# Kernel optimization log

Hardware: AMD Instinct MI355X
Metric: run time of the kernel (lower is better)

## Reference

```python
import jax, jax.numpy as jnp
import numpy as np

B, L, D, H = 2, 2048, 1024, 16
HD = D // H
SCALE = HD ** -0.5


def setup_inputs() -> dict:
    key = jax.random.key(0)
    ks = jax.random.split(key, 11)
    s = D ** -0.5  # torch Linear default init scale (uniform bound)
    return {
        "q": jax.random.normal(ks[0], (B, L, D), jnp.float32),
        "k": jax.random.normal(ks[1], (B, L, D), jnp.float32),
        "v": jax.random.normal(ks[2], (B, L, D), jnp.float32),
        "Wq": jax.random.uniform(ks[3], (D, D), jnp.float32, -s, s),
        "bq": jax.random.uniform(ks[4], (D,), jnp.float32, -s, s),
        "Wk": jax.random.uniform(ks[5], (D, D), jnp.float32, -s, s),
        "bk": jax.random.uniform(ks[6], (D,), jnp.float32, -s, s),
        "Wv": jax.random.uniform(ks[7], (D, D), jnp.float32, -s, s),
        "bv": jax.random.uniform(ks[8], (D,), jnp.float32, -s, s),
        "Wo": jax.random.uniform(ks[9], (D, D), jnp.float32, -s, s),
        "bo": jax.random.uniform(ks[10], (D,), jnp.float32, -s, s),
    }


def reference(q, k, v, Wq, bq, Wk, bk, Wv, bv, Wo, bo):
    b, q_len, _ = q.shape
    # projections; weights stored as (D, D) acting on the right: x @ W + b
    qh = (q @ Wq + bq).reshape(b, q_len, H, HD).transpose(0, 2, 1, 3)  # (B,H,Q,hd)
    kh = (k @ Wk + bk).reshape(b, -1, H, HD).transpose(0, 2, 1, 3)    # (B,H,K,hd)
    vh = (v @ Wv + bv).reshape(b, -1, H, HD).transpose(0, 2, 1, 3)    # (B,H,K,hd)
    att = jnp.einsum("bhqd,bhkd->bhqk", qh * SCALE, kh)               # (B,H,Q,K)
    att = jax.nn.softmax(att, axis=-1)
    out = jnp.einsum("bhqk,bhkd->bhqd", att, vh)                      # (B,H,Q,hd)
    out = out.transpose(0, 2, 1, 3).reshape(b, q_len, D)
    return out @ Wo + bo
```

## Files before the change

### kernel.cpp

```cpp
#include <hip/hip_runtime.h>

namespace {
constexpr int kB  = 2;
constexpr int kL  = 2048;
constexpr int kD  = 1024;
constexpr int kH  = 16;
constexpr int kHD = 64;
constexpr int kM  = kB * kL;
}

typedef _Float16 f16x8 __attribute__((ext_vector_type(8)));
typedef float    f32x16 __attribute__((ext_vector_type(16)));
typedef unsigned int u32;

union Frag16 { uint4 u4; unsigned u[4]; f16x8 v; };

__device__ __forceinline__ unsigned short f2h(float f) {
    return __builtin_bit_cast(unsigned short, (_Float16)f);
}
__device__ __forceinline__ unsigned pk2(float a, float b) {
    return __builtin_bit_cast(unsigned, __builtin_amdgcn_cvt_pkrtz(a, b));
}

__device__ __forceinline__ void gload16(const void* g, void* l) {
    __builtin_amdgcn_global_load_lds(
        (const __attribute__((address_space(1))) u32*)g,
        (__attribute__((address_space(3))) u32*)(unsigned long long)(__builtin_bit_cast(unsigned long long, l)),
        16, 0, 0);
}

__global__ __launch_bounds__(256) void prep_kernel(
    const float* __restrict__ q, const float* __restrict__ k,
    const float* __restrict__ v, unsigned short* __restrict__ dstA,
    const float* __restrict__ W0, const float* __restrict__ W1,
    const float* __restrict__ W2, const float* __restrict__ W3,
    unsigned short* __restrict__ WtBase)
{
    __shared__ _Float16 T[64][68];
    const int id = blockIdx.x;
    if (id < 6144) {
        const int yy = id >> 11;
        const int xx = id & 2047;
        const float* src = yy == 0 ? q : (yy == 1 ? k : v);
        unsigned short* d = dstA + (size_t)yy * ((size_t)kM * kD);
        const size_t i = ((size_t)xx * 256 + threadIdx.x) * 8;
        const float4 f0 = *(const float4*)(src + i);
        const float4 f1 = *(const float4*)(src + i + 4);
        _Float16 h[8];
        h[0] = (_Float16)f0.x; h[1] = (_Float16)f0.y;
        h[2] = (_Float16)f0.z; h[3] = (_Float16)f0.w;
        h[4] = (_Float16)f1.x; h[5] = (_Float16)f1.y;
        h[6] = (_Float16)f1.z; h[7] = (_Float16)f1.w;
        *(uint4*)(d + i) = *(uint4*)h;
        return;
    }
    const int id2 = id - 6144;
    const int z = id2 >> 8;
    const int rem = id2 & 255;
    const int by = rem >> 4, bx = rem & 15;
    const float* W = z == 0 ? W0 : z == 1 ? W1 : z == 2 ? W2 : W3;
    unsigned short* Wt = WtBase + (size_t)z * ((size_t)kD * kD);
    const int k0 = by * 64, n0 = bx * 64;
    const int tx = threadIdx.x & 15, ty = threadIdx.x >> 4;
#pragma unroll
    for (int i = 0; i < 4; ++i) {
        const int kk = i * 16 + ty;
        const float4 w = *(const float4*)&W[(size_t)(k0 + kk) * kD + n0 + tx * 4];
        T[tx * 4 + 0][kk] = (_Float16)w.x;
        T[tx * 4 + 1][kk] = (_Float16)w.y;
        T[tx * 4 + 2][kk] = (_Float16)w.z;
        T[tx * 4 + 3][kk] = (_Float16)w.w;
    }
    __syncthreads();
#pragma unroll
    for (int i = 0; i < 4; ++i) {
        const int nn = i * 16 + ty;
        *(ushort4*)&Wt[(size_t)(n0 + nn) * kD + k0 + tx * 4] = *(ushort4*)&T[nn][tx * 4];
    }
}

__global__ __launch_bounds__(256) void gemm_qkv_kernel(
    const unsigned short* __restrict__ A, const unsigned short* __restrict__ Wt,
    const float* __restrict__ bq, const float* __restrict__ bk,
    const float* __restrict__ bv, unsigned short* __restrict__ Qh,
    unsigned short* __restrict__ Kh, unsigned short* __restrict__ Vt)
{
    __shared__ unsigned short Als[2][128 * 64];
    __shared__ unsigned short Bls[2][128 * 64];

    const int tid = threadIdx.x;
    const int lane = tid & 63;
    const int wid = tid >> 6;
    const int l31 = lane & 31;
    const int hi = lane >> 5;
    const int by = blockIdx.x & 31;
    const int bxp = blockIdx.x >> 5;
    const int proj = bxp >> 3;
    const int bx = bxp & 7;
    const int row0 = by * 128;
    const int col0 = bx * 128;
    const int wr = wid >> 1, wc = wid & 1;

    const int rl = lane >> 3;
    const int sl = lane & 7;
    const int ssrc = (sl ^ rl) * 8;

    const unsigned short* Aproj = A + (size_t)proj * ((size_t)kM * kD);
    const unsigned short* Wproj = Wt + (size_t)proj * ((size_t)kD * kD);
    const unsigned short* Abase = Aproj + (size_t)(row0 + wid * 32 + rl) * kD + ssrc;
    const unsigned short* Bbase = Wproj + (size_t)(col0 + wid * 32 + rl) * kD + ssrc;

    f32x16 acc00{}, acc01{}, acc10{}, acc11{};

    auto stage = [&](int kt, int buf) {
#pragma unroll
        for (int i = 0; i < 4; ++i) {
            gload16(Abase + (size_t)(i * 8) * kD + kt * 64,
                    &Als[buf][(wid * 32 + i * 8) * 64]);
        }
#pragma unroll
        for (int i = 0; i < 4; ++i) {
            gload16(Bbase + (size_t)(i * 8) * kD + kt * 64,
                    &Bls[buf][(wid * 32 + i * 8) * 64]);
        }
    };

    const int ra0 = wr * 64 + l31;
    const int cb0 = wc * 64 + l31;

    stage(0, 0);
    int cur = 0;
    for (int kt = 0; kt < kD / 64; ++kt) {
        __syncthreads();
        if (kt + 1 < kD / 64) stage(kt + 1, cur ^ 1);
#pragma unroll
        for (int ks = 0; ks < 4; ++ks) {
            const int slot = (ks << 1) | hi;
            Frag16 a0, a1, b0, b1;
            a0.u4 = *(const uint4*)&Als[cur][ra0 * 64 + ((slot ^ (ra0 & 7)) << 3)];
            a1.u4 = *(const uint4*)&Als[cur][(ra0 + 32) * 64 + ((slot ^ ((ra0 + 32) & 7)) << 3)];
            b0.u4 = *(const uint4*)&Bls[cur][cb0 * 64 + ((slot ^ (cb0 & 7)) << 3)];
            b1.u4 = *(const uint4*)&Bls[cur][(cb0 + 32) * 64 + ((slot ^ ((cb0 + 32) & 7)) << 3)];
            acc00 = __builtin_amdgcn_mfma_f32_32x32x16_f16(a0.v, b0.v, acc00, 0, 0, 0);
            acc01 = __builtin_amdgcn_mfma_f32_32x32x16_f16(a0.v, b1.v, acc01, 0, 0, 0);
            acc10 = __builtin_amdgcn_mfma_f32_32x32x16_f16(a1.v, b0.v, acc10, 0, 0, 0);
            acc11 = __builtin_amdgcn_mfma_f32_32x32x16_f16(a1.v, b1.v, acc11, 0, 0, 0);
        }
        cur ^= 1;
    }

    const float* bias = proj == 0 ? bq : (proj == 1 ? bk : bv);
    const float bias0 = bias[col0 + wc * 64 + l31];
    const float bias1 = bias[col0 + wc * 64 + 32 + l31];
    const float oscale = proj == 0 ? (0.125f * 1.44269504089f) : 1.0f;

    const f32x16* accs[2][2] = {{&acc00, &acc01}, {&acc10, &acc11}};
#pragma unroll
    for (int rt = 0; rt < 2; ++rt) {
#pragma unroll
        for (int ct = 0; ct < 2; ++ct) {
            const f32x16& acv = *accs[rt][ct];
            const float bb = ct ? bias1 : bias0;
            const int c = col0 + wc * 64 + ct * 32 + l31;
            if (proj == 2) {
#pragma unroll
                for (int qd = 0; qd < 4; ++qd) {
                    const int r = row0 + wr * 64 + rt * 32 + 8 * qd + 4 * hi;
                    const int b_ = r >> 11;
                    int l_ = r & (kL - 1);
                    l_ ^= ((((l_ >> 2) ^ (l_ >> 3)) & 1) ? 12 : 0);
                    ushort4 w;
                    w.x = f2h(acv[4 * qd + 0] + bb);
                    w.y = f2h(acv[4 * qd + 1] + bb);
                    w.z = f2h(acv[4 * qd + 2] + bb);
                    w.w = f2h(acv[4 * qd + 3] + bb);
                    *(ushort4*)&Vt[((size_t)(b_ * kH + (c >> 6)) * kHD + (c & 63)) * kL + l_] = w;
                }
            } else {
                unsigned short* C = proj == 0 ? Qh : Kh;
#pragma unroll
                for (int reg = 0; reg < 16; ++reg) {
                    const int r = row0 + wr * 64 + rt * 32 + (reg & 3) + 8 * (reg >> 2) + 4 * hi;
                    const int b_ = r >> 11, l_ = r & (kL - 1);
                    C[((size_t)(b_ * kH + (c >> 6)) * kL + l_) * kHD + (c & 63)] =
                        f2h((acv[reg] + bb) * oscale);
                }
            }
        }
    }
}

__global__ __launch_bounds__(256) void gemm_o_kernel(
    const unsigned short* __restrict__ A, const unsigned short* __restrict__ Wt,
    const float* __restrict__ bias, float* __restrict__ C)
{
    __shared__ unsigned short Als[2][128 * 64];
    __shared__ unsigned short Bls[2][64 * 64];

    const int tid = threadIdx.x;
    const int lane = tid & 63;
    const int wid = tid >> 6;
    const int l31 = lane & 31;
    const int hi = lane >> 5;
    const int by = blockIdx.x & 31;
    const int bx = blockIdx.x >> 5;
    const int row0 = by * 128;
    const int wr = wid >> 1, wc = wid & 1;

    const int rl = lane >> 3;
    const int sl = lane & 7;
    const int ssrc = (sl ^ rl) * 8;

    const unsigned short* Abase = A + (size_t)(row0 + wid * 32 + rl) * kD + ssrc;
    const unsigned short* Bbase = Wt + (size_t)(bx * 64 + wid * 16 + rl) * kD + ssrc;

    f32x16 acc0{}, acc1{};

    auto stage = [&](int kt, int buf) {
#pragma unroll
        for (int i = 0; i < 4; ++i)
            gload16(Abase + (size_t)(i * 8) * kD + kt * 64,
                    &Als[buf][(wid * 32 + i * 8) * 64]);
        gload16(Bbase + kt * 64,                   &Bls[buf][(wid * 16) * 64]);
        gload16(Bbase + (size_t)8 * kD + kt * 64,  &Bls[buf][(wid * 16 + 8) * 64]);
    };

    const int ra0 = wr * 64 + l31;
    const int cb0 = wc * 32 + l31;

    stage(0, 0);
    int cur = 0;
    for (int kt = 0; kt < kD / 64; ++kt) {
        __syncthreads();
        if (kt + 1 < kD / 64) stage(kt + 1, cur ^ 1);
#pragma unroll
        for (int ks = 0; ks < 4; ++ks) {
            const int slot = (ks << 1) | hi;
            Frag16 a0, a1, b0;
            a0.u4 = *(const uint4*)&Als[cur][ra0 * 64 + ((slot ^ (ra0 & 7)) << 3)];
            a1.u4 = *(const uint4*)&Als[cur][(ra0 + 32) * 64 + ((slot ^ ((ra0 + 32) & 7)) << 3)];
            b0.u4 = *(const uint4*)&Bls[cur][cb0 * 64 + ((slot ^ (cb0 & 7)) << 3)];
            acc0 = __builtin_amdgcn_mfma_f32_32x32x16_f16(a0.v, b0.v, acc0, 0, 0, 0);
            acc1 = __builtin_amdgcn_mfma_f32_32x32x16_f16(a1.v, b0.v, acc1, 0, 0, 0);
        }
        cur ^= 1;
    }

    const int c = (bx << 6) + wc * 32 + l31;
    const float bb = bias[c];
    const f32x16* accs[2] = {&acc0, &acc1};
#pragma unroll
    for (int rt = 0; rt < 2; ++rt) {
        const f32x16& acv = *accs[rt];
#pragma unroll
        for (int reg = 0; reg < 16; ++reg) {
            const int r = row0 + wr * 64 + rt * 32 + (reg & 3) + 8 * (reg >> 2) + 4 * hi;
            C[(size_t)r * kD + c] = acv[reg] + bb;
        }
    }
}

__global__ __launch_bounds__(512) void attn_mfma_kernel(
    const unsigned short* __restrict__ Qh, const unsigned short* __restrict__ Kh,
    const unsigned short* __restrict__ Vt, unsigned short* __restrict__ Opart,
    float2* __restrict__ Stat)
{
    __shared__ unsigned short Kls[4][64 * 64];
    __shared__ unsigned short Vls[4][64 * 64];

    const int lane = threadIdx.x & 63;
    const int wid  = threadIdx.x >> 6;
    const int l31  = lane & 31;
    const int hi   = lane >> 5;

    const int id = blockIdx.x;
    const int j  = id >> 3;
    const int bh = (id & 7) * 4 + (j >> 4);
    const int qt = j & 7;
    const int ks = (j >> 3) & 1;
    const int q = qt * 256 + wid * 32 + l31;

    const size_t qkBase = (size_t)bh * kL * kHD;
    const unsigned short* Qp = Qh + qkBase + (size_t)q * kHD + hi * 8;
    Frag16 qf[4];
#pragma unroll
    for (int d = 0; d < 4; ++d) qf[d].u4 = *(const uint4*)(Qp + d * 16);

    const int srow = wid * 8 + (lane >> 3);
    const int soff = (((lane & 7) ^ (srow & 7)) << 3);
    const unsigned short* Kg = Kh + qkBase + (size_t)srow * kHD + soff;
    const unsigned short* Vg = Vt + (size_t)bh * kHD * kL + (size_t)srow * kL + soff;

    auto stage = [&](int kt, int buf) {
        gload16(Kg + (size_t)(kt * 64) * kHD, &Kls[buf][(wid * 8) * 64]);
        gload16(Vg + kt * 64,                 &Vls[buf][(wid * 8) * 64]);
    };

    f32x16 o0{}, o1{};
    float lsum = 0.f;
    const int rA = l31, rB = l31 + 32;

    const int kt0 = ks * 16;
    stage(kt0 + 0, 0);
    stage(kt0 + 1, 1);

    for (int rt = 0; rt < 8; ++rt) {
        const int t0 = 2 * rt;
        asm volatile("s_waitcnt vmcnt(0)" ::: "memory");
        __builtin_amdgcn_s_barrier();
        if (t0 + 3 < 16) {
            stage(kt0 + t0 + 2, (t0 + 2) & 3);
            stage(kt0 + t0 + 3, (t0 + 3) & 3);
        }
        const int bA = t0 & 3, bB = (t0 + 1) & 3;

        f32x16 c0{}, c1{}, c2{}, c3{};
        __builtin_amdgcn_s_setprio(1);
#pragma unroll
        for (int d = 0; d < 4; ++d) {
            const int s = (d << 1) | hi;
            Frag16 ka0, ka1, kb0, kb1;
            ka0.u4 = *(const uint4*)&Kls[bA][rA * 64 + ((s ^ (rA & 7)) << 3)];
            ka1.u4 = *(const uint4*)&Kls[bA][rB * 64 + ((s ^ (rB & 7)) << 3)];
            kb0.u4 = *(const uint4*)&Kls[bB][rA * 64 + ((s ^ (rA & 7)) << 3)];
            kb1.u4 = *(const uint4*)&Kls[bB][rB * 64 + ((s ^ (rB & 7)) << 3)];
            c0 = __builtin_amdgcn_mfma_f32_32x32x16_f16(ka0.v, qf[d].v, c0, 0, 0, 0);
            c1 = __builtin_amdgcn_mfma_f32_32x32x16_f16(ka1.v, qf[d].v, c1, 0, 0, 0);
            c2 = __builtin_amdgcn_mfma_f32_32x32x16_f16(kb0.v, qf[d].v, c2, 0, 0, 0);
            c3 = __builtin_amdgcn_mfma_f32_32x32x16_f16(kb1.v, qf[d].v, c3, 0, 0, 0);
        }
        __builtin_amdgcn_s_setprio(0);

        Frag16 vA0[4], vA1[4];
#pragma unroll
        for (int ksl = 0; ksl < 4; ++ksl) {
            const int s = (ksl << 1) | hi;
            vA0[ksl].u4 = *(const uint4*)&Vls[bA][rA * 64 + ((s ^ (rA & 7)) << 3)];
            vA1[ksl].u4 = *(const uint4*)&Vls[bA][rB * 64 + ((s ^ (rB & 7)) << 3)];
        }

        float rs = 0.f;
        Frag16 pfA[4];
#pragma unroll
        for (int i = 0; i < 8; ++i) {
            const float e0 = __builtin_amdgcn_exp2f(c0[2 * i]);
            const float e1 = __builtin_amdgcn_exp2f(c0[2 * i + 1]);
            const float e2 = __builtin_amdgcn_exp2f(c1[2 * i]);
            const float e3 = __builtin_amdgcn_exp2f(c1[2 * i + 1]);
            pfA[i >> 2].u[i & 3]       = pk2(e0, e1);
            pfA[2 + (i >> 2)].u[i & 3] = pk2(e2, e3);
            rs += (e0 + e1) + (e2 + e3);
        }

        Frag16 pfB[4];
        __builtin_amdgcn_s_setprio(1);
#pragma unroll
        for (int ksl = 0; ksl < 4; ++ksl) {
            o0 = __builtin_amdgcn_mfma_f32_32x32x16_f16(vA0[ksl].v, pfA[ksl].v, o0, 0, 0, 0);
            o1 = __builtin_amdgcn_mfma_f32_32x32x16_f16(vA1[ksl].v, pfA[ksl].v, o1, 0, 0, 0);
        }
        __builtin_amdgcn_s_setprio(0);
#pragma unroll
        for (int i = 0; i < 8; ++i) {
            const float e4 = __builtin_amdgcn_exp2f(c2[2 * i]);
            const float e5 = __builtin_amdgcn_exp2f(c2[2 * i + 1]);
            const float e6 = __builtin_amdgcn_exp2f(c3[2 * i]);
            const float e7 = __builtin_amdgcn_exp2f(c3[2 * i + 1]);
            pfB[i >> 2].u[i & 3]       = pk2(e4, e5);
            pfB[2 + (i >> 2)].u[i & 3] = pk2(e6, e7);
            rs += (e4 + e5) + (e6 + e7);
        }
        rs += __shfl_xor(rs, 32);
        lsum += rs;

        __builtin_amdgcn_s_setprio(1);
#pragma unroll
        for (int ksl = 0; ksl < 4; ++ksl) {
            const int s = (ksl << 1) | hi;
            Frag16 v0, v1;
            v0.u4 = *(const uint4*)&Vls[bB][rA * 64 + ((s ^ (rA & 7)) << 3)];
            v1.u4 = *(const uint4*)&Vls[bB][rB * 64 + ((s ^ (rB & 7)) << 3)];
            o0 = __builtin_amdgcn_mfma_f32_32x32x16_f16(v0.v, pfB[ksl].v, o0, 0, 0, 0);
            o1 = __builtin_amdgcn_mfma_f32_32x32x16_f16(v1.v, pfB[ksl].v, o1, 0, 0, 0);
        }
        __builtin_amdgcn_s_setprio(0);
    }

    const size_t prow = (size_t)ks * (32 * kL) + (size_t)bh * kL + q;
    const float inv = 1.f / lsum;
    unsigned short* pp = Opart + prow * kHD;
#pragma unroll
    for (int g = 0; g < 4; ++g) {
        const int d = g * 8 + hi * 4;
        uint2 w0, w1;
        w0.x = pk2(o0[4 * g + 0] * inv, o0[4 * g + 1] * inv);
        w0.y = pk2(o0[4 * g + 2] * inv, o0[4 * g + 3] * inv);
        w1.x = pk2(o1[4 * g + 0] * inv, o1[4 * g + 1] * inv);
        w1.y = pk2(o1[4 * g + 2] * inv, o1[4 * g + 3] * inv);
        *(uint2*)(pp + d) = w0;
        *(uint2*)(pp + 32 + d) = w1;
    }
    if (hi == 0) Stat[prow] = make_float2(0.f, lsum);
}

__global__ __launch_bounds__(256) void merge_kernel(
    const unsigned short* __restrict__ Opart, const float2* __restrict__ Stat,
    unsigned short* __restrict__ O16)
{
    const int g = blockIdx.x * 256 + threadIdx.x;
    const int row = g >> 3;
    const int d0 = (g & 7) * 8;
    const int bh = row >> 11, q = row & (kL - 1);
    const float2 sa = Stat[row];
    const float2 sb = Stat[32 * kL + row];
    float wa = sa.y;
    float wb = sb.y;
    const float inv = 1.f / (wa + wb);
    wa *= inv; wb *= inv;

    const unsigned short* pa = Opart + (size_t)row * kHD + d0;
    const unsigned short* pb = pa + (size_t)32 * kL * kHD;
    uint4 ua = *(const uint4*)pa;
    uint4 ub = *(const uint4*)pb;
    _Float16 ha[8], hb[8];
    *(uint4*)ha = ua;
    *(uint4*)hb = ub;
    unsigned out[4];
#pragma unroll
    for (int i = 0; i < 4; ++i) {
        const float v0 = wa * (float)ha[2 * i]     + wb * (float)hb[2 * i];
        const float v1 = wa * (float)ha[2 * i + 1] + wb * (float)hb[2 * i + 1];
        out[i] = pk2(v0, v1);
    }
    const int b_ = bh >> 4, h_ = bh & 15;
    *(uint4*)&O16[((size_t)(b_ * kL + q)) * kD + h_ * kHD + d0] = *(uint4*)out;
}

extern "C" void kernel_launch(void* const* d_in, const int* in_sizes, int n_in,
                              void* d_out, int out_size, void* d_ws, size_t ws_size,
                              hipStream_t stream)
{
    const float* q  = (const float*)d_in[0];
    const float* k  = (const float*)d_in[1];
    const float* v  = (const float*)d_in[2];
    const float* Wq = (const float*)d_in[3];
    const float* bq = (const float*)d_in[4];
    const float* Wk = (const float*)d_in[5];
    const float* bk = (const float*)d_in[6];
    const float* Wv = (const float*)d_in[7];
    const float* bv = (const float*)d_in[8];
    const float* Wo = (const float*)d_in[9];
    const float* bo = (const float*)d_in[10];
    float* out = (float*)d_out;

    const size_t MD = (size_t)kM * kD;
    const size_t DD = (size_t)kD * kD;
    unsigned short* A16 = (unsigned short*)d_ws;
    unsigned short* Wt16 = A16 + 3 * MD;
    unsigned short* Qh16 = Wt16 + 4 * DD;
    unsigned short* Kh16 = Qh16 + MD;
    unsigned short* Vt16 = Kh16 + MD;
    unsigned short* O16   = A16;
    unsigned short* Opart = A16 + MD;
    float2*         Stat  = (float2*)Wt16;

    const dim3 blk(256);

    hipLaunchKernelGGL(prep_kernel, dim3(7168), blk, 0, stream,
                       q, k, v, A16, Wq, Wk, Wv, Wo, Wt16);

    hipLaunchKernelGGL(gemm_qkv_kernel, dim3(32 * 24), blk, 0, stream,
                       A16, Wt16, bq, bk, bv, Qh16, Kh16, Vt16);

    hipLaunchKernelGGL(attn_mfma_kernel, dim3(512), dim3(512), 0, stream,
                       Qh16, Kh16, Vt16, Opart, Stat);
    hipLaunchKernelGGL(merge_kernel, dim3(2048), blk, 0, stream,
                       Opart, Stat, O16);

    hipLaunchKernelGGL(gemm_o_kernel, dim3(32 * 16), blk, 0, stream,
                       O16, Wt16 + 3 * DD, bo, out);
}
```

Measured before the change: 120.4 us.

## Fuse split-K attention merge into output projection GEMM A-tile load

Removes the separate merge kernel. The output-projection GEMM now reads both split-K attention partials and their row sums directly, blends them in registers, and writes the merged fp16 A tile into shared memory. That write happens after the MFMA loop so the loads overlap with compute. This drops one kernel launch and an intermediate global round-trip. In exchange, each GEMM column block redoes the merge, reading twice as much A data and running extra ALU work. Separately, the attention kernel hoists the second V-fragment LDS loads ahead of the exp computation to hide LDS latency, at the cost of more registers.

```diff
diff --git a/kernel.cpp b/kernel.cpp
--- a/kernel.cpp
+++ b/kernel.cpp
@@ -191,8 +191,9 @@
 }
 
 __global__ __launch_bounds__(256) void gemm_o_kernel(
-    const unsigned short* __restrict__ A, const unsigned short* __restrict__ Wt,
-    const float* __restrict__ bias, float* __restrict__ C)
+    const unsigned short* __restrict__ Opart, const float2* __restrict__ Stat,
+    const unsigned short* __restrict__ Wt, const float* __restrict__ bias,
+    float* __restrict__ C)
 {
     __shared__ unsigned short Als[2][128 * 64];
     __shared__ unsigned short Bls[2][64 * 64];
@@ -211,28 +212,64 @@
     const int sl = lane & 7;
     const int ssrc = (sl ^ rl) * 8;
 
-    const unsigned short* Abase = A + (size_t)(row0 + wid * 32 + rl) * kD + ssrc;
     const unsigned short* Bbase = Wt + (size_t)(bx * 64 + wid * 16 + rl) * kD + ssrc;
 
     f32x16 acc0{}, acc1{};
 
-    auto stage = [&](int kt, int buf) {
-#pragma unroll
-        for (int i = 0; i < 4; ++i)
-            gload16(Abase + (size_t)(i * 8) * kD + kt * 64,
-                    &Als[buf][(wid * 32 + i * 8) * 64]);
+    auto stageB = [&](int kt, int buf) {
         gload16(Bbase + kt * 64,                   &Bls[buf][(wid * 16) * 64]);
         gload16(Bbase + (size_t)8 * kD + kt * 64,  &Bls[buf][(wid * 16 + 8) * 64]);
     };
 
+    uint4 pa_[4], pb_[4];
+    float2 sa_[4], sb_[4];
+    auto loadA = [&](int kt) {
+#pragma unroll
+        for (int i = 0; i < 4; ++i) {
+            const int grow = row0 + wid * 32 + i * 8 + rl;
+            const int b_ = grow >> 11, l_ = grow & (kL - 1);
+            const int bhq = (b_ * kH + kt) * kL + l_;
+            const unsigned short* pa = Opart + (size_t)bhq * kHD + ssrc;
+            pa_[i] = *(const uint4*)pa;
+            pb_[i] = *(const uint4*)(pa + (size_t)32 * kL * kHD);
+            sa_[i] = Stat[bhq];
+            sb_[i] = Stat[32 * kL + bhq];
+        }
+    };
+    auto writeA = [&](int buf) {
+#pragma unroll
+        for (int i = 0; i < 4; ++i) {
+            const float inv = 1.f / (sa_[i].y + sb_[i].y);
+            const float wa = sa_[i].y * inv, wb = sb_[i].y * inv;
+            _Float16 ha[8], hb[8];
+            *(uint4*)ha = pa_[i];
+            *(uint4*)hb = pb_[i];
+            uint4 w;
+            w.x = pk2(wa * (float)ha[0] + wb * (float)hb[0],
+                      wa * (float)ha[1] + wb * (float)hb[1]);
+            w.y = pk2(wa * (float)ha[2] + wb * (float)hb[2],
+                      wa * (float)ha[3] + wb * (float)hb[3]);
+            w.z = pk2(wa * (float)ha[4] + wb * (float)hb[4],
+                      wa * (float)ha[5] + wb * (float)hb[5]);
+            w.w = pk2(wa * (float)ha[6] + wb * (float)hb[6],
+                      wa * (float)ha[7] + wb * (float)hb[7]);
+            *(uint4*)&Als[buf][(wid * 32 + i * 8 + rl) * 64 + sl * 8] = w;
+        }
+    };
+
     const int ra0 = wr * 64 + l31;
     const int cb0 = wc * 32 + l31;
 
-    stage(0, 0);
+    loadA(0);
+    stageB(0, 0);
+    writeA(0);
     int cur = 0;
     for (int kt = 0; kt < kD / 64; ++kt) {
         __syncthreads();
-        if (kt + 1 < kD / 64) stage(kt + 1, cur ^ 1);
+        if (kt + 1 < kD / 64) {
+            loadA(kt + 1);
+            stageB(kt + 1, cur ^ 1);
+        }
 #pragma unroll
         for (int ks = 0; ks < 4; ++ks) {
             const int slot = (ks << 1) | hi;
@@ -243,6 +280,7 @@
             acc0 = __builtin_amdgcn_mfma_f32_32x32x16_f16(a0.v, b0.v, acc0, 0, 0, 0);
             acc1 = __builtin_amdgcn_mfma_f32_32x32x16_f16(a1.v, b0.v, acc1, 0, 0, 0);
         }
+        if (kt + 1 < kD / 64) writeA(cur ^ 1);
         cur ^= 1;
     }
 
@@ -352,7 +390,6 @@
             rs += (e0 + e1) + (e2 + e3);
         }
 
-        Frag16 pfB[4];
         __builtin_amdgcn_s_setprio(1);
 #pragma unroll
         for (int ksl = 0; ksl < 4; ++ksl) {
@@ -360,6 +397,16 @@
             o1 = __builtin_amdgcn_mfma_f32_32x32x16_f16(vA1[ksl].v, pfA[ksl].v, o1, 0, 0, 0);
         }
         __builtin_amdgcn_s_setprio(0);
+
+        Frag16 vB0[4], vB1[4];
+#pragma unroll
+        for (int ksl = 0; ksl < 4; ++ksl) {
+            const int s = (ksl << 1) | hi;
+            vB0[ksl].u4 = *(const uint4*)&Vls[bB][rA * 64 + ((s ^ (rA & 7)) << 3)];
+            vB1[ksl].u4 = *(const uint4*)&Vls[bB][rB * 64 + ((s ^ (rB & 7)) << 3)];
+        }
+
+        Frag16 pfB[4];
 #pragma unroll
         for (int i = 0; i < 8; ++i) {
             const float e4 = __builtin_amdgcn_exp2f(c2[2 * i]);
@@ -376,12 +423,8 @@
         __builtin_amdgcn_s_setprio(1);
 #pragma unroll
         for (int ksl = 0; ksl < 4; ++ksl) {
-            const int s = (ksl << 1) | hi;
-            Frag16 v0, v1;
-            v0.u4 = *(const uint4*)&Vls[bB][rA * 64 + ((s ^ (rA & 7)) << 3)];
-            v1.u4 = *(const uint4*)&Vls[bB][rB * 64 + ((s ^ (rB & 7)) << 3)];
-            o0 = __builtin_amdgcn_mfma_f32_32x32x16_f16(v0.v, pfB[ksl].v, o0, 0, 0, 0);
-            o1 = __builtin_amdgcn_mfma_f32_32x32x16_f16(v1.v, pfB[ksl].v, o1, 0, 0, 0);
+            o0 = __builtin_amdgcn_mfma_f32_32x32x16_f16(vB0[ksl].v, pfB[ksl].v, o0, 0, 0, 0);
+            o1 = __builtin_amdgcn_mfma_f32_32x32x16_f16(vB1[ksl].v, pfB[ksl].v, o1, 0, 0, 0);
         }
         __builtin_amdgcn_s_setprio(0);
     }
@@ -401,39 +444,6 @@
         *(uint2*)(pp + 32 + d) = w1;
     }
     if (hi == 0) Stat[prow] = make_float2(0.f, lsum);
-}
-
-__global__ __launch_bounds__(256) void merge_kernel(
-    const unsigned short* __restrict__ Opart, const float2* __restrict__ Stat,
-    unsigned short* __restrict__ O16)
-{
-    const int g = blockIdx.x * 256 + threadIdx.x;
-    const int row = g >> 3;
-    const int d0 = (g & 7) * 8;
-    const int bh = row >> 11, q = row & (kL - 1);
-    const float2 sa = Stat[row];
-    const float2 sb = Stat[32 * kL + row];
-    float wa = sa.y;
-    float wb = sb.y;
-    const float inv = 1.f / (wa + wb);
-    wa *= inv; wb *= inv;
-
-    const unsigned short* pa = Opart + (size_t)row * kHD + d0;
-    const unsigned short* pb = pa + (size_t)32 * kL * kHD;
-    uint4 ua = *(const uint4*)pa;
-    uint4 ub = *(const uint4*)pb;
-    _Float16 ha[8], hb[8];
-    *(uint4*)ha = ua;
-    *(uint4*)hb = ub;
-    unsigned out[4];
-#pragma unroll
-    for (int i = 0; i < 4; ++i) {
-        const float v0 = wa * (float)ha[2 * i]     + wb * (float)hb[2 * i];
-        const float v1 = wa * (float)ha[2 * i + 1] + wb * (float)hb[2 * i + 1];
-        out[i] = pk2(v0, v1);
-    }
-    const int b_ = bh >> 4, h_ = bh & 15;
-    *(uint4*)&O16[((size_t)(b_ * kL + q)) * kD + h_ * kHD + d0] = *(uint4*)out;
 }
 
 extern "C" void kernel_launch(void* const* d_in, const int* in_sizes, int n_in,
@@ -460,7 +470,6 @@
     unsigned short* Qh16 = Wt16 + 4 * DD;
     unsigned short* Kh16 = Qh16 + MD;
     unsigned short* Vt16 = Kh16 + MD;
-    unsigned short* O16   = A16;
     unsigned short* Opart = A16 + MD;
     float2*         Stat  = (float2*)Wt16;
 
@@ -474,9 +483,7 @@
 
     hipLaunchKernelGGL(attn_mfma_kernel, dim3(512), dim3(512), 0, stream,
                        Qh16, Kh16, Vt16, Opart, Stat);
-    hipLaunchKernelGGL(merge_kernel, dim3(2048), blk, 0, stream,
-                       Opart, Stat, O16);
 
     hipLaunchKernelGGL(gemm_o_kernel, dim3(32 * 16), blk, 0, stream,
-                       O16, Wt16 + 3 * DD, bo, out);
-}
+                       Opart, Stat, Wt16 + 3 * DD, bo, out);
+}
```

Measured after the change: 124.2 us. 1.03x slower.
